# Kernel tuning notes

Hardware: AMD Instinct MI355X
Metric: run time of the kernel (lower is better)

Reference implementation:

```python
import jax, jax.numpy as jnp
import numpy as np
from itertools import combinations

NDIM = 256
BATCH = 65536


def setup_inputs() -> dict:
    key = jax.random.key(0)
    k1, k2 = jax.random.split(key)
    pairs = np.array(list(combinations(range(NDIM), 2)), dtype=np.int32)  # [comb(ndim,2), 2]
    return {
        "x": jax.random.normal(k1, (BATCH, NDIM), dtype=jnp.float32),
        "rots": jax.random.normal(k2, (pairs.shape[0],), dtype=jnp.float32),
        "idx_i": jnp.asarray(pairs[:, 0]),
        "idx_j": jnp.asarray(pairs[:, 1]),
    }


def _build_mat(rots, idx_i, idx_j, ndim):
    # Equivalent to mat = R_last @ ... @ R_first @ I, then return mat.T.
    # Each Givens rotation R_(i,j,theta) only mixes rows i and j, so we update
    # two rows per step (O(ndim) work) instead of a dense ndim x ndim matmul.
    # Torch uses cfloat, but all imaginary parts are identically zero, so
    # float32 computes the same math.
    def step(mat, t):
        i, j, theta = t
        c = jnp.cos(theta)
        s = jnp.sin(theta)
        ri = mat[i]
        rj = mat[j]
        mat = mat.at[i].set(c * ri - s * rj)
        mat = mat.at[j].set(s * ri + c * rj)
        return mat, None

    mat0 = jnp.eye(ndim, dtype=rots.dtype)
    mat, _ = jax.lax.scan(step, mat0, (idx_i, idx_j, rots))
    return mat.T  # forward does x @ mat.T


def reference(x, rots, idx_i, idx_j):
    m = _build_mat(rots, idx_i, idx_j, x.shape[-1])  # [ndim, ndim]
    return x @ m
```

## Files before the change

### kernel.cpp

```cpp
#include <hip/hip_runtime.h>
#include <hip/hip_bf16.h>
#include <math.h>

#define NDIM 256
#define NROT 32640
#define NSEG 64
#define SEGLEN 510
#define MATE (NDIM * NDIM)
#define NODEE (2 * MATE)

typedef __bf16 bf16x4_t __attribute__((ext_vector_type(4)));
typedef __bf16 bf16x8_t __attribute__((ext_vector_type(8)));
typedef float f32x4_t __attribute__((ext_vector_type(4)));


#define ROT1(RJ, CS) { float nri_ = fmaf((CS).x, ri, -((CS).y * (RJ))); \
                       (RJ) = fmaf((CS).y, ri, (CS).x * (RJ)); ri = nri_; }

#define LOAD16(P, JB, KK) \
    P##0 = *(const f32x4_t*)&tile[(JB)][t][0]; \
    P##1 = *(const f32x4_t*)&tile[(JB)][t][4]; \
    P##2 = *(const f32x4_t*)&tile[(JB) + 1][t][0]; \
    P##3 = *(const f32x4_t*)&tile[(JB) + 1][t][4]; \
    _Pragma("unroll") \
    for (int u = 0; u < 16; u++) P##c[u] = csl[(KK) + u];

#define COMP16(P, JB) \
    _Pragma("unroll") \
    for (int u = 0; u < 4; u++) ROT1(P##0[u], P##c[u]) \
    _Pragma("unroll") \
    for (int u = 0; u < 4; u++) ROT1(P##1[u], P##c[4 + u]) \
    _Pragma("unroll") \
    for (int u = 0; u < 4; u++) ROT1(P##2[u], P##c[8 + u]) \
    _Pragma("unroll") \
    for (int u = 0; u < 4; u++) ROT1(P##3[u], P##c[12 + u]) \
    *(f32x4_t*)&tile[(JB)][t][0] = P##0; \
    *(f32x4_t*)&tile[(JB)][t][4] = P##1; \
    *(f32x4_t*)&tile[(JB) + 1][t][0] = P##2; \
    *(f32x4_t*)&tile[(JB) + 1][t][4] = P##3;

__global__ __launch_bounds__(64, 1) void k_build(const float* __restrict__ rots,
                                                 __bf16* __restrict__ leaves) {
    __shared__ float tile[32][64][8];
    __shared__ float2 csl[SEGLEN + 16];
    const int t = threadIdx.x;
    const int seg = blockIdx.x >> 2;
    const int cg = blockIdx.x & 3;
    const int col = cg * 64 + t;
    const int kg0 = seg * SEGLEN;

    for (int u = t; u < SEGLEN; u += 64) {
        float th = rots[kg0 + u];
        float s, c;
        sincosf(th, &s, &c);
        csl[u] = make_float2(c, s);
    }
    for (int u = SEGLEN + t; u < SEGLEN + 16; u += 64) csl[u] = make_float2(1.f, 0.f);

    #pragma unroll
    for (int jb = 0; jb < 32; jb++) {
        f32x4_t z0 = {0.f, 0.f, 0.f, 0.f}, z1 = {0.f, 0.f, 0.f, 0.f};
        if ((col >> 3) == jb) {
            if ((col & 7) < 4) z0[col & 3] = 1.0f;
            else               z1[col & 3] = 1.0f;
        }
        *(f32x4_t*)&tile[jb][t][0] = z0;
        *(f32x4_t*)&tile[jb][t][4] = z1;
    }

    int k = 0;
    int i = 0, cum = 0;
    while (cum + (NDIM - 1 - i) <= kg0) { cum += NDIM - 1 - i; i++; }
    int j = i + 1 + (kg0 - cum);

    float* T = &tile[0][0][0];
    #define TADDR(r) ((((r) >> 3) * 512) + t * 8 + ((r) & 7))

    while (k < SEGLEN) {
        float ri = T[TADDR(i)];
        int rem = min(NDIM - j, SEGLEN - k);

        int npeel = min((8 - (j & 7)) & 7, rem);
        for (int u = 0; u < npeel; u++) {
            float2 cs = csl[k];
            float rj = T[TADDR(j)];
            float nri = fmaf(cs.x, ri, -(cs.y * rj));
            T[TADDR(j)] = fmaf(cs.y, ri, cs.x * rj);
            ri = nri; j++; k++;
        }
        rem -= npeel;

        if (rem >= 16) {
            int jb = j >> 3;
            f32x4_t A0, A1, A2, A3, B0, B1, B2, B3;
            float2 Ac[16], Bc[16];
            LOAD16(A, jb, k)
            while (rem >= 48) {
                LOAD16(B, jb + 2, k + 16)
                COMP16(A, jb)
                jb += 2; j += 16; k += 16; rem -= 16;
                LOAD16(A, jb + 2, k + 16)
                COMP16(B, jb)
                jb += 2; j += 16; k += 16; rem -= 16;
            }
            if (rem >= 32) {
                LOAD16(B, jb + 2, k + 16)
                COMP16(A, jb)
                jb += 2; j += 16; k += 16; rem -= 16;
                COMP16(B, jb)
                jb += 2; j += 16; k += 16; rem -= 16;
            } else {
                COMP16(A, jb)
                jb += 2; j += 16; k += 16; rem -= 16;
            }
        }

        if (rem >= 8) {
            int jb = j >> 3;
            f32x4_t a0 = *(const f32x4_t*)&tile[jb][t][0];
            f32x4_t a1 = *(const f32x4_t*)&tile[jb][t][4];
            float2 cc[8];
            #pragma unroll
            for (int u = 0; u < 8; u++) cc[u] = csl[k + u];
            #pragma unroll
            for (int u = 0; u < 4; u++) ROT1(a0[u], cc[u])
            #pragma unroll
            for (int u = 0; u < 4; u++) ROT1(a1[u], cc[4 + u])
            *(f32x4_t*)&tile[jb][t][0] = a0;
            *(f32x4_t*)&tile[jb][t][4] = a1;
            j += 8; k += 8; rem -= 8;
        }

        while (rem > 0) {
            float2 cs = csl[k];
            float rj = T[TADDR(j)];
            float nri = fmaf(cs.x, ri, -(cs.y * rj));
            T[TADDR(j)] = fmaf(cs.y, ri, cs.x * rj);
            ri = nri; j++; k++; rem--;
        }

        T[TADDR(i)] = ri;
        if (j == NDIM) { i++; j = i + 1; }
    }
    #undef TADDR

    __bf16* hi = leaves + (size_t)seg * NODEE;
    __bf16* lo = hi + MATE;
    if (seg & 1) {
        for (int jb = 0; jb < 32; jb++) {
            f32x4_t v0 = *(const f32x4_t*)&tile[jb][t][0];
            f32x4_t v1 = *(const f32x4_t*)&tile[jb][t][4];
            #pragma unroll
            for (int u = 0; u < 8; u++) {
                float v = (u < 4) ? v0[u & 3] : v1[u & 3];
                __bf16 h = (__bf16)v;
                hi[(size_t)(jb * 8 + u) * NDIM + col] = h;
                lo[(size_t)(jb * 8 + u) * NDIM + col] = (__bf16)(v - (float)h);
            }
        }
    } else {
        for (int jb = 0; jb < 32; jb++) {
            f32x4_t v0 = *(const f32x4_t*)&tile[jb][t][0];
            f32x4_t v1 = *(const f32x4_t*)&tile[jb][t][4];
            bf16x8_t vh, vl;
            #pragma unroll
            for (int u = 0; u < 8; u++) {
                float v = (u < 4) ? v0[u & 3] : v1[u & 3];
                __bf16 h = (__bf16)v;
                vh[u] = h;
                vl[u] = (__bf16)(v - (float)h);
            }
            *(bf16x8_t*)&hi[(size_t)col * NDIM + jb * 8] = vh;
            *(bf16x8_t*)&lo[(size_t)col * NDIM + jb * 8] = vl;
        }
    }
}

#define LDK 264
__global__ __launch_bounds__(256) void k_combine(const __bf16* __restrict__ src,
                                                 __bf16* __restrict__ dst,
                                                 int finalLevel) {
    __shared__ __bf16 planes[4][64 * LDK];

    const int p = blockIdx.x >> 4;
    const int qd = blockIdx.x & 15;
    const int rbq = (qd >> 2) * 64;
    const int cbq = (qd & 3) * 64;
    const __bf16* A = src + (size_t)(2 * p) * NODEE;
    const __bf16* B = src + (size_t)(2 * p + 1) * NODEE;
    __bf16* Chi = dst + (size_t)p * NODEE;
    __bf16* Clo = Chi + MATE;
    const bool storeT = (!finalLevel) && ((p & 1) == 0);

    const int t = threadIdx.x;
    const int wid = t >> 6, lane = t & 63;
    const int wr2 = (wid >> 1) * 32, wc2 = (wid & 1) * 32;
    const int lrow = lane & 15, kg = lane >> 4;

    const __bf16* plane_src[4] = {B, B + MATE, A, A + MATE};
    const int plane_row0[4] = {rbq, rbq, cbq, cbq};
    #pragma unroll
    for (int q = 0; q < 32; q++) {
        int g = q * 256 + t;
        int pl = g >> 11;
        int c = g & 2047;
        int row = c >> 5, sg = c & 31;
        bf16x8_t v = *(const bf16x8_t*)&plane_src[pl][(size_t)(plane_row0[pl] + row) * NDIM + sg * 8];
        *(bf16x8_t*)&planes[pl][row * LDK + sg * 8] = v;
    }
    __syncthreads();

    f32x4_t acc[2][2] = {};
    #pragma unroll
    for (int kc = 0; kc < 8; kc++) {
        bf16x8_t afh[2], afl[2], bfh[2], bfl[2];
        #pragma unroll
        for (int mt = 0; mt < 2; mt++) {
            int r = (wr2 + mt * 16 + lrow) * LDK + kc * 32 + kg * 8;
            afh[mt] = *(const bf16x8_t*)&planes[0][r];
            afl[mt] = *(const bf16x8_t*)&planes[1][r];
        }
        #pragma unroll
        for (int nt = 0; nt < 2; nt++) {
            int r = (wc2 + nt * 16 + lrow) * LDK + kc * 32 + kg * 8;
            bfh[nt] = *(const bf16x8_t*)&planes[2][r];
            bfl[nt] = *(const bf16x8_t*)&planes[3][r];
        }
        #pragma unroll
        for (int mt = 0; mt < 2; mt++)
            #pragma unroll
            for (int nt = 0; nt < 2; nt++) {
                acc[mt][nt] = __builtin_amdgcn_mfma_f32_16x16x32_bf16(afh[mt], bfh[nt], acc[mt][nt], 0, 0, 0);
                acc[mt][nt] = __builtin_amdgcn_mfma_f32_16x16x32_bf16(afh[mt], bfl[nt], acc[mt][nt], 0, 0, 0);
                acc[mt][nt] = __builtin_amdgcn_mfma_f32_16x16x32_bf16(afl[mt], bfh[nt], acc[mt][nt], 0, 0, 0);
            }
    }

    #pragma unroll
    for (int mt = 0; mt < 2; mt++)
        #pragma unroll
        for (int nt = 0; nt < 2; nt++) {
            int grow = rbq + wr2 + mt * 16 + kg * 4;
            int gcol = cbq + wc2 + nt * 16 + lrow;
            if (storeT) {
                bf16x4_t vh, vl;
                #pragma unroll
                for (int r = 0; r < 4; r++) {
                    float v = acc[mt][nt][r];
                    __bf16 h = (__bf16)v;
                    vh[r] = h;
                    vl[r] = (__bf16)(v - (float)h);
                }
                *(bf16x4_t*)&Chi[(size_t)gcol * NDIM + grow] = vh;
                *(bf16x4_t*)&Clo[(size_t)gcol * NDIM + grow] = vl;
            } else if (finalLevel) {
                #pragma unroll
                for (int r = 0; r < 4; r++)
                    Chi[(size_t)(grow + r) * NDIM + gcol] = (__bf16)acc[mt][nt][r];
            } else {
                #pragma unroll
                for (int r = 0; r < 4; r++) {
                    float v = acc[mt][nt][r];
                    __bf16 h = (__bf16)v;
                    Chi[(size_t)(grow + r) * NDIM + gcol] = h;
                    Clo[(size_t)(grow + r) * NDIM + gcol] = (__bf16)(v - (float)h);
                }
            }
        }
}

#define LDA 72
__global__ __launch_bounds__(256, 2) void k_gemm(const float* __restrict__ X,
                                                 const __bf16* __restrict__ Mhi,
                                                 float* __restrict__ Y) {
    __shared__ __bf16 As[128 * LDA];
    __shared__ __bf16 Bs[128 * LDA];
    const int bx = blockIdx.x;
    const int xcd = bx & 7;
    const int q = bx >> 3;
    const int bn = (q & 1) * 128;
    const int bm = (xcd + (q >> 1) * 8) * 128;
    const int t = threadIdx.x;
    const int wid = t >> 6;
    const int lane = t & 63;
    const int wr = (wid >> 1) * 64;
    const int wc = (wid & 1) * 64;
    const int lrow = lane & 15;
    const int kg = lane >> 4;

    f32x4_t acc[4][4] = {};

    f32x4_t ra[8];
    bf16x8_t rb[4];

    #pragma unroll
    for (int qq = 0; qq < 8; qq++) {
        int g = qq * 256 + t;
        ra[qq] = *(const f32x4_t*)&X[(size_t)(bm + (g >> 4)) * 256 + (g & 15) * 4];
    }
    #pragma unroll
    for (int qq = 0; qq < 4; qq++) {
        int g = qq * 256 + t;
        rb[qq] = *(const bf16x8_t*)&Mhi[(size_t)(bn + (g >> 3)) * 256 + (g & 7) * 8];
    }

    #pragma unroll
    for (int it = 0; it < 4; it++) {
        #pragma unroll
        for (int qq = 0; qq < 8; qq++) {
            int g = qq * 256 + t;
            f32x4_t v = ra[qq];
            bf16x4_t h = {(__bf16)v.x, (__bf16)v.y, (__bf16)v.z, (__bf16)v.w};
            *(bf16x4_t*)&As[(g >> 4) * LDA + (g & 15) * 4] = h;
        }
        #pragma unroll
        for (int qq = 0; qq < 4; qq++) {
            int g = qq * 256 + t;
            *(bf16x8_t*)&Bs[(g >> 3) * LDA + (g & 7) * 8] = rb[qq];
        }
        __syncthreads();

        if (it < 3) {
            int kc = (it + 1) * 64;
            #pragma unroll
            for (int qq = 0; qq < 8; qq++) {
                int g = qq * 256 + t;
                ra[qq] = *(const f32x4_t*)&X[(size_t)(bm + (g >> 4)) * 256 + kc + (g & 15) * 4];
            }
            #pragma unroll
            for (int qq = 0; qq < 4; qq++) {
                int g = qq * 256 + t;
                rb[qq] = *(const bf16x8_t*)&Mhi[(size_t)(bn + (g >> 3)) * 256 + kc + (g & 7) * 8];
            }
        }

        #pragma unroll
        for (int k2 = 0; k2 < 2; k2++) {
            bf16x8_t af[4], bfr[4];
            #pragma unroll
            for (int mt = 0; mt < 4; mt++)
                af[mt] = *(const bf16x8_t*)&As[(wr + mt * 16 + lrow) * LDA + k2 * 32 + kg * 8];
            #pragma unroll
            for (int nt = 0; nt < 4; nt++)
                bfr[nt] = *(const bf16x8_t*)&Bs[(wc + nt * 16 + lrow) * LDA + k2 * 32 + kg * 8];
            #pragma unroll
            for (int mt = 0; mt < 4; mt++)
                #pragma unroll
                for (int nt = 0; nt < 4; nt++)
                    acc[mt][nt] = __builtin_amdgcn_mfma_f32_16x16x32_bf16(af[mt], bfr[nt], acc[mt][nt], 0, 0, 0);
        }
        __syncthreads();
    }

    const int ocol = bn + wc + lrow;
    const int orow = bm + wr + kg * 4;
    #pragma unroll
    for (int mt = 0; mt < 4; mt++)
        #pragma unroll
        for (int nt = 0; nt < 4; nt++)
            #pragma unroll
            for (int r = 0; r < 4; r++)
                Y[(size_t)(orow + mt * 16 + r) * 256 + ocol + nt * 16] = acc[mt][nt][r];
}

extern "C" void kernel_launch(void* const* d_in, const int* in_sizes, int n_in,
                              void* d_out, int out_size, void* d_ws, size_t ws_size,
                              hipStream_t stream) {
    const float* x = (const float*)d_in[0];
    const float* rots = (const float*)d_in[1];
    float* out = (float*)d_out;

    __bf16* B0 = (__bf16*)d_ws;
    __bf16* B1 = B0 + (size_t)NSEG * NODEE;

    k_build<<<NSEG * 4, 64, 0, stream>>>(rots, B0);
    k_combine<<<32 * 16, 256, 0, stream>>>(B0, B1, 0);
    k_combine<<<16 * 16, 256, 0, stream>>>(B1, B0, 0);
    k_combine<<<8 * 16, 256, 0, stream>>>(B0, B1, 0);
    k_combine<<<4 * 16, 256, 0, stream>>>(B1, B0, 0);
    k_combine<<<2 * 16, 256, 0, stream>>>(B0, B1, 0);
    k_combine<<<1 * 16, 256, 0, stream>>>(B1, B0, 1);
    k_gemm<<<1024, 256, 0, stream>>>(x, B0, out);
}
```

Measured before the change: 222.5 us.

## Split build segments on row boundaries with cost balancing; use direct global-to-LDS loads

Build segments now start and end on whole rotation rows. Each segment's boundaries come from a binary search over a cost model with a fixed per-row cost plus a per-rotation cost, so segments hold uneven rotation counts chosen to balance time. This drops the mid-row start logic and wrapping, and should cut peel and tail overhead because every row starts at i+1. Separately, the combine kernel stages its operand planes with global_load_lds straight into unpadded shared memory. That removes the register round-trip but gives up the LDK padding, which risks bank conflicts on the MFMA fragment reads.

```diff
diff --git a/kernel.cpp b/kernel.cpp
--- a/kernel.cpp
+++ b/kernel.cpp
@@ -5,13 +5,19 @@
 #define NDIM 256
 #define NROT 32640
 #define NSEG 64
-#define SEGLEN 510
 #define MATE (NDIM * NDIM)
 #define NODEE (2 * MATE)
+
+#define BF 1280
+#define BC 16
+#define CSLMAX 1104
 
 typedef __bf16 bf16x4_t __attribute__((ext_vector_type(4)));
 typedef __bf16 bf16x8_t __attribute__((ext_vector_type(8)));
 typedef float f32x4_t __attribute__((ext_vector_type(4)));
+
+typedef __attribute__((address_space(1))) const unsigned int g_u32;
+typedef __attribute__((address_space(3))) unsigned int l_u32;
 
 
 #define ROT1(RJ, CS) { float nri_ = fmaf((CS).x, ri, -((CS).y * (RJ))); \
@@ -39,23 +45,45 @@
     *(f32x4_t*)&tile[(JB) + 1][t][0] = P##2; \
     *(f32x4_t*)&tile[(JB) + 1][t][4] = P##3;
 
+__device__ __forceinline__ int run_off(int r) {
+    return 255 * r - (r * (r - 1)) / 2;
+}
+__device__ __forceinline__ int cum_cost(int r) {
+    return BF * r + BC * run_off(r);
+}
+__device__ __forceinline__ int seg_boundary(int s) {
+    if (s <= 0) return 0;
+    if (s >= NSEG) return 255;
+    const long target = ((long)cum_cost(255) * s) / NSEG;
+    int lo = 0, hi = 255;
+    while (lo < hi) {
+        int mid = (lo + hi) >> 1;
+        if ((long)cum_cost(mid) >= target) hi = mid; else lo = mid + 1;
+    }
+    return lo;
+}
+
 __global__ __launch_bounds__(64, 1) void k_build(const float* __restrict__ rots,
                                                  __bf16* __restrict__ leaves) {
     __shared__ float tile[32][64][8];
-    __shared__ float2 csl[SEGLEN + 16];
+    __shared__ float2 csl[CSLMAX];
     const int t = threadIdx.x;
     const int seg = blockIdx.x >> 2;
-    const int cg = blockIdx.x & 3;
-    const int col = cg * 64 + t;
-    const int kg0 = seg * SEGLEN;
-
-    for (int u = t; u < SEGLEN; u += 64) {
+    const int cg_ = blockIdx.x & 3;
+    const int col = cg_ * 64 + t;
+
+    const int r0 = seg_boundary(seg);
+    const int r1 = seg_boundary(seg + 1);
+    const int kg0 = run_off(r0);
+    const int nrot = run_off(r1) - kg0;
+
+    for (int u = t; u < nrot; u += 64) {
         float th = rots[kg0 + u];
         float s, c;
         sincosf(th, &s, &c);
         csl[u] = make_float2(c, s);
     }
-    for (int u = SEGLEN + t; u < SEGLEN + 16; u += 64) csl[u] = make_float2(1.f, 0.f);
+    for (int u = nrot + t; u < nrot + 16 && u < CSLMAX; u += 64) csl[u] = make_float2(1.f, 0.f);
 
     #pragma unroll
     for (int jb = 0; jb < 32; jb++) {
@@ -68,17 +96,14 @@
         *(f32x4_t*)&tile[jb][t][4] = z1;
     }
 
-    int k = 0;
-    int i = 0, cum = 0;
-    while (cum + (NDIM - 1 - i) <= kg0) { cum += NDIM - 1 - i; i++; }
-    int j = i + 1 + (kg0 - cum);
-
     float* T = &tile[0][0][0];
     #define TADDR(r) ((((r) >> 3) * 512) + t * 8 + ((r) & 7))
 
-    while (k < SEGLEN) {
+    int k = 0;
+    for (int i = r0; i < r1; ++i) {
         float ri = T[TADDR(i)];
-        int rem = min(NDIM - j, SEGLEN - k);
+        int j = i + 1;
+        int rem = NDIM - j;
 
         int npeel = min((8 - (j & 7)) & 7, rem);
         for (int u = 0; u < npeel; u++) {
@@ -140,7 +165,6 @@
         }
 
         T[TADDR(i)] = ri;
-        if (j == NDIM) { i++; j = i + 1; }
     }
     #undef TADDR
 
@@ -176,11 +200,10 @@
     }
 }
 
-#define LDK 264
 __global__ __launch_bounds__(256) void k_combine(const __bf16* __restrict__ src,
                                                  __bf16* __restrict__ dst,
                                                  int finalLevel) {
-    __shared__ __bf16 planes[4][64 * LDK];
+    __shared__ __align__(16) __bf16 planes[4][64 * 256];
 
     const int p = blockIdx.x >> 4;
     const int qd = blockIdx.x & 15;
@@ -199,14 +222,17 @@
 
     const __bf16* plane_src[4] = {B, B + MATE, A, A + MATE};
     const int plane_row0[4] = {rbq, rbq, cbq, cbq};
-    #pragma unroll
-    for (int q = 0; q < 32; q++) {
-        int g = q * 256 + t;
-        int pl = g >> 11;
-        int c = g & 2047;
-        int row = c >> 5, sg = c & 31;
-        bf16x8_t v = *(const bf16x8_t*)&plane_src[pl][(size_t)(plane_row0[pl] + row) * NDIM + sg * 8];
-        *(bf16x8_t*)&planes[pl][row * LDK + sg * 8] = v;
+
+    {
+        const __bf16* gsrc = plane_src[wid] + (size_t)plane_row0[wid] * NDIM + lane * 8;
+        __bf16* lbase = &planes[wid][0];
+        #pragma unroll
+        for (int W = 0; W < 32; W++) {
+            __builtin_amdgcn_global_load_lds(
+                (g_u32*)(gsrc + W * 512),
+                (l_u32*)(lbase + W * 512),
+                16, 0, 0);
+        }
     }
     __syncthreads();
 
@@ -216,13 +242,13 @@
         bf16x8_t afh[2], afl[2], bfh[2], bfl[2];
         #pragma unroll
         for (int mt = 0; mt < 2; mt++) {
-            int r = (wr2 + mt * 16 + lrow) * LDK + kc * 32 + kg * 8;
+            int r = (wr2 + mt * 16 + lrow) * 256 + kc * 32 + kg * 8;
             afh[mt] = *(const bf16x8_t*)&planes[0][r];
             afl[mt] = *(const bf16x8_t*)&planes[1][r];
         }
         #pragma unroll
         for (int nt = 0; nt < 2; nt++) {
-            int r = (wc2 + nt * 16 + lrow) * LDK + kc * 32 + kg * 8;
+            int r = (wc2 + nt * 16 + lrow) * 256 + kc * 32 + kg * 8;
             bfh[nt] = *(const bf16x8_t*)&planes[2][r];
             bfl[nt] = *(const bf16x8_t*)&planes[3][r];
         }
```

Measured after the change: 214.8 us. -3.5%, faster.
